# Optimization experiments

Measured on AMD Instinct MI355X. Metric: run time of the kernel, lower is better.

## Reference

```python
import jax, jax.numpy as jnp
import numpy as np

NUM_FEATURES = 128
NUM_FILTERS = 128

def setup_inputs() -> dict:
    key = jax.random.key(0)
    k1, k2, k3, k4, k5 = jax.random.split(key, 5)
    B, N, F = 4, 2048, NUM_FEATURES
    x = jax.random.normal(k1, (B, N, F), dtype=jnp.float32)
    A = jax.random.normal(k2, (B, N, N), dtype=jnp.float32)
    # Conv1D(num_filters, kernel_size=1, use_bias=False) == per-node linear F -> filters
    W = jax.random.normal(k3, (F, NUM_FILTERS), dtype=jnp.float32) * (1.0 / np.sqrt(F))
    # self.a: Conv1D(1, kernel_size=1) with bias == linear filters -> 1 (shared for x_i and x_j)
    a_w = jax.random.normal(k4, (NUM_FILTERS, 1), dtype=jnp.float32) * (1.0 / np.sqrt(NUM_FILTERS))
    a_b = jax.random.normal(k5, (1,), dtype=jnp.float32) * 0.01
    bias = jnp.zeros((NUM_FILTERS,), dtype=jnp.float32)
    return {"x": x, "A": A, "W": W, "a_w": a_w, "a_b": a_b, "bias": bias}

def reference(x, A, W, a_w, a_b, bias):
    # project features: [B,N,F] @ [F,Ff] -> [B,N,Ff]
    h = jnp.einsum('bnf,fg->bng', x, W)
    # shared attention projection (x_i and x_j use the same layer): [B,N,1]
    s = jnp.einsum('bng,go->bno', h, a_w) + a_b
    # additive scores s_i + s_j^T -> [B,N,N]
    e = s + jnp.swapaxes(s, 1, 2)
    e = jnp.where(e >= 0, e, 0.2 * e)  # LeakyReLU(0.2)
    attn = jax.nn.softmax(e + A, axis=-1)
    out = jnp.einsum('bij,bjg->big', attn, h) + bias
    return out
```

## Files before the change

kernel.cpp:

```cpp
#include <hip/hip_runtime.h>
#include <hip/hip_bf16.h>
#include <stdint.h>

#define BB 4
#define NN 2048
#define FF 128

typedef __attribute__((ext_vector_type(8))) short bf16x8;
typedef __attribute__((ext_vector_type(4))) float f32x4;

__device__ inline unsigned pk_bf16(float a, float b) {
    union { float f; unsigned u; } x, y;
    x.f = a; y.f = b;
    unsigned xu = x.u + (0x7fffu + ((x.u >> 16) & 1u));
    unsigned yu = y.u + (0x7fffu + ((y.u >> 16) & 1u));
    return (xu >> 16) | (yu & 0xffff0000u);
}

#define XT_P 136
#define WT_P 136

__global__ __launch_bounds__(256) void k1_proj(
    const float* __restrict__ x, const float* __restrict__ W,
    const float* __restrict__ a_w, const float* __restrict__ a_b,
    uint16_t* __restrict__ Ht, float* __restrict__ s_out)
{
    __shared__ uint16_t xt[16 * XT_P];
    __shared__ uint16_t Wt[128 * WT_P];
    __shared__ float sredw[4 * 16];

    const int t = threadIdx.x;
    const int w = t >> 6, l = t & 63;
    const int m16 = l & 15, q = l >> 4;
    const int b = blockIdx.x >> 7;
    const int n0 = (blockIdx.x & 127) << 4;

    const int c4 = (t & 31) * 4, kh = (t >> 5) * 16;
    float4 wr0[8], wr1[8];
    #pragma unroll
    for (int kk = 0; kk < 8; ++kk) {
        const int k = kh + 2 * kk;
        wr0[kk] = *(const float4*)(W + (size_t)k * 128 + c4);
        wr1[kk] = *(const float4*)(W + (size_t)(k + 1) * 128 + c4);
    }
    {
        const int row = t >> 4, c0 = (t & 15) * 8;
        const float* xr = x + ((size_t)(b * NN + n0 + row)) * FF + c0;
        const float4 v0 = *(const float4*)xr;
        const float4 v1 = *(const float4*)(xr + 4);
        unsigned* dst = (unsigned*)(xt + row * XT_P + c0);
        dst[0] = pk_bf16(v0.x, v0.y); dst[1] = pk_bf16(v0.z, v0.w);
        dst[2] = pk_bf16(v1.x, v1.y); dst[3] = pk_bf16(v1.z, v1.w);
    }
    #pragma unroll
    for (int kk = 0; kk < 8; ++kk) {
        const int k = kh + 2 * kk;
        *(unsigned*)(Wt + (c4 + 0) * WT_P + k) = pk_bf16(wr0[kk].x, wr1[kk].x);
        *(unsigned*)(Wt + (c4 + 1) * WT_P + k) = pk_bf16(wr0[kk].y, wr1[kk].y);
        *(unsigned*)(Wt + (c4 + 2) * WT_P + k) = pk_bf16(wr0[kk].z, wr1[kk].z);
        *(unsigned*)(Wt + (c4 + 3) * WT_P + k) = pk_bf16(wr0[kk].w, wr1[kk].w);
    }
    const int g0 = (2 * w) * 16 + m16, g1 = (2 * w + 1) * 16 + m16;
    const float aw0 = a_w[g0], aw1 = a_w[g1];
    __syncthreads();

    f32x4 acc0 = {}, acc1 = {};
    bf16x8 af[4];
    #pragma unroll
    for (int dk = 0; dk < 4; ++dk)
        af[dk] = *(const bf16x8*)(xt + m16 * XT_P + dk * 32 + q * 8);
    #pragma unroll
    for (int dk = 0; dk < 4; ++dk) {
        bf16x8 b0 = *(const bf16x8*)(Wt + g0 * WT_P + dk * 32 + q * 8);
        bf16x8 b1 = *(const bf16x8*)(Wt + g1 * WT_P + dk * 32 + q * 8);
        acc0 = __builtin_amdgcn_mfma_f32_16x16x32_bf16(af[dk], b0, acc0, 0, 0, 0);
        acc1 = __builtin_amdgcn_mfma_f32_16x16x32_bf16(af[dk], b1, acc1, 0, 0, 0);
    }

    float sp[4];
    #pragma unroll
    for (int r = 0; r < 4; ++r) sp[r] = acc0[r] * aw0 + acc1[r] * aw1;
    #pragma unroll
    for (int off = 1; off < 16; off <<= 1)
        #pragma unroll
        for (int r = 0; r < 4; ++r) sp[r] += __shfl_xor(sp[r], off, 64);
    if (m16 == 0) {
        #pragma unroll
        for (int r = 0; r < 4; ++r) sredw[w * 16 + q * 4 + r] = sp[r];
    }
    {
        uint2 o0 = { pk_bf16(acc0[0], acc0[1]), pk_bf16(acc0[2], acc0[3]) };
        uint2 o1 = { pk_bf16(acc1[0], acc1[1]), pk_bf16(acc1[2], acc1[3]) };
        *(uint2*)(Ht + ((size_t)(b * 128 + g0)) * NN + n0 + q * 4) = o0;
        *(uint2*)(Ht + ((size_t)(b * 128 + g1)) * NN + n0 + q * 4) = o1;
    }
    __syncthreads();
    if (t < 16)
        s_out[b * NN + n0 + t] = sredw[t] + sredw[16 + t] + sredw[32 + t] + sredw[48 + t] + a_b[0];
}

__global__ __launch_bounds__(256, 2) void k2_attn(
    const float* __restrict__ A, const uint16_t* __restrict__ Ht,
    const float* __restrict__ s, const float* __restrict__ bias,
    float* __restrict__ out)
{
    __shared__ float Opw[4][16 * 132];
    __shared__ float rsw[4][16];

    const int t = threadIdx.x;
    const int w = t >> 6, l = t & 63;
    const int m16 = l & 15, q = l >> 4;

    const int is = blockIdx.x & 127;
    const int b  = blockIdx.x >> 7;
    const int ibase = is * 16;

    const float* sb = s + b * NN;
    const float* Ab = A + (size_t)b * NN * NN;
    const uint16_t* Hb = Ht + (size_t)b * FF * NN;

    const float si = sb[ibase + m16];
    const float* Ar = Ab + (size_t)(ibase + m16) * NN;

    const int co = w * 32 + q * 8;

    float4 a00 = *(const float4*)(Ar + co);
    float4 a01 = *(const float4*)(Ar + co + 4);
    float4 a10 = *(const float4*)(Ar + co + 128);
    float4 a11 = *(const float4*)(Ar + co + 132);
    float4 sj00 = *(const float4*)(sb + co);
    float4 sj01 = *(const float4*)(sb + co + 4);
    float4 sj10 = *(const float4*)(sb + co + 128);
    float4 sj11 = *(const float4*)(sb + co + 132);

    f32x4 acc[8];
    #pragma unroll
    for (int gt = 0; gt < 8; ++gt) acc[gt] = (f32x4){0.f, 0.f, 0.f, 0.f};
    float rs = 0.f;

    #pragma unroll
    for (int r = 0; r < 8; ++r) {
        const int jc0 = r * 256 + co;
        const int jc1 = jc0 + 128;

        bf16x8 hf0[8], hf1[8];
        #pragma unroll
        for (int gt = 0; gt < 8; ++gt) {
            const uint16_t* hp = Hb + (size_t)(gt * 16 + m16) * NN;
            hf0[gt] = *(const bf16x8*)(hp + jc0);
            hf1[gt] = *(const bf16x8*)(hp + jc1);
        }

        float4 n00, n01, n10, n11, t00, t01, t10, t11;
        if (r < 7) {
            const int jn = jc0 + 256;
            n00 = *(const float4*)(Ar + jn);
            n01 = *(const float4*)(Ar + jn + 4);
            n10 = *(const float4*)(Ar + jn + 128);
            n11 = *(const float4*)(Ar + jn + 132);
            t00 = *(const float4*)(sb + jn);
            t01 = *(const float4*)(sb + jn + 4);
            t10 = *(const float4*)(sb + jn + 128);
            t11 = *(const float4*)(sb + jn + 132);
        }

        const float svv[16] = {sj00.x,sj00.y,sj00.z,sj00.w, sj01.x,sj01.y,sj01.z,sj01.w,
                               sj10.x,sj10.y,sj10.z,sj10.w, sj11.x,sj11.y,sj11.z,sj11.w};
        const float avv[16] = {a00.x,a00.y,a00.z,a00.w, a01.x,a01.y,a01.z,a01.w,
                               a10.x,a10.y,a10.z,a10.w, a11.x,a11.y,a11.z,a11.w};
        float pv[16];
        #pragma unroll
        for (int j = 0; j < 16; ++j) {
            float e = si + svv[j];
            e = fmaxf(e, 0.2f * e);
            pv[j] = __expf(e + avv[j]);
            rs += pv[j];
        }
        union { unsigned u[4]; bf16x8 v; } fa0, fa1;
        #pragma unroll
        for (int j = 0; j < 4; ++j) {
            fa0.u[j] = pk_bf16(pv[2 * j], pv[2 * j + 1]);
            fa1.u[j] = pk_bf16(pv[8 + 2 * j], pv[9 + 2 * j]);
        }

        #pragma unroll
        for (int gt = 0; gt < 8; ++gt) {
            acc[gt] = __builtin_amdgcn_mfma_f32_16x16x32_bf16(fa0.v, hf0[gt], acc[gt], 0, 0, 0);
            acc[gt] = __builtin_amdgcn_mfma_f32_16x16x32_bf16(fa1.v, hf1[gt], acc[gt], 0, 0, 0);
        }

        if (r < 7) {
            a00 = n00; a01 = n01; a10 = n10; a11 = n11;
            sj00 = t00; sj01 = t01; sj10 = t10; sj11 = t11;
        }
    }

    rs += __shfl_xor(rs, 16, 64);
    rs += __shfl_xor(rs, 32, 64);
    if (q == 0) rsw[w][m16] = rs;
    #pragma unroll
    for (int gt = 0; gt < 8; ++gt)
        #pragma unroll
        for (int rr = 0; rr < 4; ++rr)
            Opw[w][(q * 4 + rr) * 132 + gt * 16 + m16] = acc[gt][rr];
    __syncthreads();

    {
        const int row = t >> 4, k8 = (t & 15) * 8;
        float v[8] = {0.f,0.f,0.f,0.f,0.f,0.f,0.f,0.f};
        #pragma unroll
        for (int sl = 0; sl < 4; ++sl) {
            float4 u0 = *(const float4*)&Opw[sl][row * 132 + k8];
            float4 u1 = *(const float4*)&Opw[sl][row * 132 + k8 + 4];
            v[0] += u0.x; v[1] += u0.y; v[2] += u0.z; v[3] += u0.w;
            v[4] += u1.x; v[5] += u1.y; v[6] += u1.z; v[7] += u1.w;
        }
        const float rst = rsw[0][row] + rsw[1][row] + rsw[2][row] + rsw[3][row];
        const float inv = 1.0f / rst;
        const float4 b0 = *(const float4*)(bias + k8);
        const float4 b1 = *(const float4*)(bias + k8 + 4);
        float4 o0 = { v[0]*inv + b0.x, v[1]*inv + b0.y, v[2]*inv + b0.z, v[3]*inv + b0.w };
        float4 o1 = { v[4]*inv + b1.x, v[5]*inv + b1.y, v[6]*inv + b1.z, v[7]*inv + b1.w };
        float* op = out + ((size_t)(b * NN + ibase + row)) * FF + k8;
        *(float4*)op = o0;
        *(float4*)(op + 4) = o1;
    }
}

extern "C" void kernel_launch(void* const* d_in, const int* in_sizes, int n_in,
                              void* d_out, int out_size, void* d_ws, size_t ws_size,
                              hipStream_t stream) {
    const float* x    = (const float*)d_in[0];
    const float* A    = (const float*)d_in[1];
    const float* W    = (const float*)d_in[2];
    const float* a_w  = (const float*)d_in[3];
    const float* a_b  = (const float*)d_in[4];
    const float* bias = (const float*)d_in[5];
    float* out = (float*)d_out;

    char* ws = (char*)d_ws;
    uint16_t* Ht = (uint16_t*)ws;
    float* s = (float*)(ws + 2 * 1024 * 1024);

    k1_proj<<<BB * (NN / 16), 256, 0, stream>>>(x, W, a_w, a_b, Ht, s);
    k2_attn<<<128 * BB, 256, 0, stream>>>(A, Ht, s, bias, out);
}
```

Baseline: 138.7 us.

## Split attention K-loop across eight waves per block with two-stage LDS reduction

The attention kernel now runs 512 threads (8 waves) per block, and each wave handles one 8-column chunk per 256-column stripe instead of two, halving per-wave registers and loop work. The explicit software prefetch of A and s is dropped, the block index is remapped so that batches are interleaved, and partial outputs are reduced through LDS in two phases (upper waves store, lower waves accumulate) so the buffer size stays the same. The aim is more waves in flight to hide the latency of streaming A. The cost is an extra barrier and the loss of explicit prefetching.

```diff
diff --git a/kernel.cpp b/kernel.cpp
--- a/kernel.cpp
+++ b/kernel.cpp
@@ -99,20 +99,20 @@
         s_out[b * NN + n0 + t] = sredw[t] + sredw[16 + t] + sredw[32 + t] + sredw[48 + t] + a_b[0];
 }
 
-__global__ __launch_bounds__(256, 2) void k2_attn(
+__global__ __launch_bounds__(512, 4) void k2_attn(
     const float* __restrict__ A, const uint16_t* __restrict__ Ht,
     const float* __restrict__ s, const float* __restrict__ bias,
     float* __restrict__ out)
 {
     __shared__ float Opw[4][16 * 132];
-    __shared__ float rsw[4][16];
+    __shared__ float rsw[8][16];
 
     const int t = threadIdx.x;
     const int w = t >> 6, l = t & 63;
     const int m16 = l & 15, q = l >> 4;
 
-    const int is = blockIdx.x & 127;
-    const int b  = blockIdx.x >> 7;
+    const int b  = blockIdx.x & 3;
+    const int is = blockIdx.x >> 2;
     const int ibase = is * 16;
 
     const float* sb = s + b * NN;
@@ -121,17 +121,9 @@
 
     const float si = sb[ibase + m16];
     const float* Ar = Ab + (size_t)(ibase + m16) * NN;
+    const uint16_t* Hr = Hb + (size_t)m16 * NN;
 
     const int co = w * 32 + q * 8;
-
-    float4 a00 = *(const float4*)(Ar + co);
-    float4 a01 = *(const float4*)(Ar + co + 4);
-    float4 a10 = *(const float4*)(Ar + co + 128);
-    float4 a11 = *(const float4*)(Ar + co + 132);
-    float4 sj00 = *(const float4*)(sb + co);
-    float4 sj01 = *(const float4*)(sb + co + 4);
-    float4 sj10 = *(const float4*)(sb + co + 128);
-    float4 sj11 = *(const float4*)(sb + co + 132);
 
     f32x4 acc[8];
     #pragma unroll
@@ -139,91 +131,76 @@
     float rs = 0.f;
 
     #pragma unroll
-    for (int r = 0; r < 8; ++r) {
-        const int jc0 = r * 256 + co;
-        const int jc1 = jc0 + 128;
-
-        bf16x8 hf0[8], hf1[8];
-        #pragma unroll
-        for (int gt = 0; gt < 8; ++gt) {
-            const uint16_t* hp = Hb + (size_t)(gt * 16 + m16) * NN;
-            hf0[gt] = *(const bf16x8*)(hp + jc0);
-            hf1[gt] = *(const bf16x8*)(hp + jc1);
-        }
-
-        float4 n00, n01, n10, n11, t00, t01, t10, t11;
-        if (r < 7) {
-            const int jn = jc0 + 256;
-            n00 = *(const float4*)(Ar + jn);
-            n01 = *(const float4*)(Ar + jn + 4);
-            n10 = *(const float4*)(Ar + jn + 128);
-            n11 = *(const float4*)(Ar + jn + 132);
-            t00 = *(const float4*)(sb + jn);
-            t01 = *(const float4*)(sb + jn + 4);
-            t10 = *(const float4*)(sb + jn + 128);
-            t11 = *(const float4*)(sb + jn + 132);
-        }
-
-        const float svv[16] = {sj00.x,sj00.y,sj00.z,sj00.w, sj01.x,sj01.y,sj01.z,sj01.w,
-                               sj10.x,sj10.y,sj10.z,sj10.w, sj11.x,sj11.y,sj11.z,sj11.w};
-        const float avv[16] = {a00.x,a00.y,a00.z,a00.w, a01.x,a01.y,a01.z,a01.w,
-                               a10.x,a10.y,a10.z,a10.w, a11.x,a11.y,a11.z,a11.w};
-        float pv[16];
-        #pragma unroll
-        for (int j = 0; j < 16; ++j) {
-            float e = si + svv[j];
+    for (int hr = 0; hr < 8; ++hr) {
+        const int jc = hr * 256 + co;
+
+        bf16x8 hf[8];
+        #pragma unroll
+        for (int gt = 0; gt < 8; ++gt)
+            hf[gt] = *(const bf16x8*)(Hr + (size_t)(gt * 16) * NN + jc);
+
+        float4 a0 = *(const float4*)(Ar + jc);
+        float4 a1 = *(const float4*)(Ar + jc + 4);
+        float4 s0 = *(const float4*)(sb + jc);
+        float4 s1 = *(const float4*)(sb + jc + 4);
+
+        const float sv[8] = {s0.x, s0.y, s0.z, s0.w, s1.x, s1.y, s1.z, s1.w};
+        const float av[8] = {a0.x, a0.y, a0.z, a0.w, a1.x, a1.y, a1.z, a1.w};
+        float pv[8];
+        #pragma unroll
+        for (int j = 0; j < 8; ++j) {
+            float e = si + sv[j];
             e = fmaxf(e, 0.2f * e);
-            pv[j] = __expf(e + avv[j]);
+            pv[j] = __expf(e + av[j]);
             rs += pv[j];
         }
-        union { unsigned u[4]; bf16x8 v; } fa0, fa1;
-        #pragma unroll
-        for (int j = 0; j < 4; ++j) {
-            fa0.u[j] = pk_bf16(pv[2 * j], pv[2 * j + 1]);
-            fa1.u[j] = pk_bf16(pv[8 + 2 * j], pv[9 + 2 * j]);
-        }
-
-        #pragma unroll
-        for (int gt = 0; gt < 8; ++gt) {
-            acc[gt] = __builtin_amdgcn_mfma_f32_16x16x32_bf16(fa0.v, hf0[gt], acc[gt], 0, 0, 0);
-            acc[gt] = __builtin_amdgcn_mfma_f32_16x16x32_bf16(fa1.v, hf1[gt], acc[gt], 0, 0, 0);
-        }
-
-        if (r < 7) {
-            a00 = n00; a01 = n01; a10 = n10; a11 = n11;
-            sj00 = t00; sj01 = t01; sj10 = t10; sj11 = t11;
-        }
+        union { unsigned u[4]; bf16x8 v; } fa;
+        #pragma unroll
+        for (int j = 0; j < 4; ++j)
+            fa.u[j] = pk_bf16(pv[2 * j], pv[2 * j + 1]);
+
+        #pragma unroll
+        for (int gt = 0; gt < 8; ++gt)
+            acc[gt] = __builtin_amdgcn_mfma_f32_16x16x32_bf16(fa.v, hf[gt], acc[gt], 0, 0, 0);
     }
 
     rs += __shfl_xor(rs, 16, 64);
     rs += __shfl_xor(rs, 32, 64);
     if (q == 0) rsw[w][m16] = rs;
-    #pragma unroll
-    for (int gt = 0; gt < 8; ++gt)
-        #pragma unroll
-        for (int rr = 0; rr < 4; ++rr)
-            Opw[w][(q * 4 + rr) * 132 + gt * 16 + m16] = acc[gt][rr];
+
+    if (w >= 4) {
+        #pragma unroll
+        for (int gt = 0; gt < 8; ++gt)
+            #pragma unroll
+            for (int rr = 0; rr < 4; ++rr)
+                Opw[w - 4][(q * 4 + rr) * 132 + gt * 16 + m16] = acc[gt][rr];
+    }
+    __syncthreads();
+    if (w < 4) {
+        #pragma unroll
+        for (int gt = 0; gt < 8; ++gt)
+            #pragma unroll
+            for (int rr = 0; rr < 4; ++rr)
+                Opw[w][(q * 4 + rr) * 132 + gt * 16 + m16] += acc[gt][rr];
+    }
     __syncthreads();
 
     {
-        const int row = t >> 4, k8 = (t & 15) * 8;
-        float v[8] = {0.f,0.f,0.f,0.f,0.f,0.f,0.f,0.f};
+        const int row = t >> 5, k4 = (t & 31) * 4;
+        float4 v = {0.f, 0.f, 0.f, 0.f};
         #pragma unroll
         for (int sl = 0; sl < 4; ++sl) {
-            float4 u0 = *(const float4*)&Opw[sl][row * 132 + k8];
-            float4 u1 = *(const float4*)&Opw[sl][row * 132 + k8 + 4];
-            v[0] += u0.x; v[1] += u0.y; v[2] += u0.z; v[3] += u0.w;
-            v[4] += u1.x; v[5] += u1.y; v[6] += u1.z; v[7] += u1.w;
+            float4 u = *(const float4*)&Opw[sl][row * 132 + k4];
+            v.x += u.x; v.y += u.y; v.z += u.z; v.w += u.w;
         }
-        const float rst = rsw[0][row] + rsw[1][row] + rsw[2][row] + rsw[3][row];
+        float rst = 0.f;
+        #pragma unroll
+        for (int sl = 0; sl < 8; ++sl) rst += rsw[sl][row];
         const float inv = 1.0f / rst;
-        const float4 b0 = *(const float4*)(bias + k8);
-        const float4 b1 = *(const float4*)(bias + k8 + 4);
-        float4 o0 = { v[0]*inv + b0.x, v[1]*inv + b0.y, v[2]*inv + b0.z, v[3]*inv + b0.w };
-        float4 o1 = { v[4]*inv + b1.x, v[5]*inv + b1.y, v[6]*inv + b1.z, v[7]*inv + b1.w };
-        float* op = out + ((size_t)(b * NN + ibase + row)) * FF + k8;
-        *(float4*)op = o0;
-        *(float4*)(op + 4) = o1;
+        const float4 bv = *(const float4*)(bias + k4);
+        float4 o = { v.x * inv + bv.x, v.y * inv + bv.y,
+                     v.z * inv + bv.z, v.w * inv + bv.w };
+        *(float4*)(out + ((size_t)(b * NN + ibase + row)) * FF + k4) = o;
     }
 }
 
@@ -243,5 +220,5 @@
     float* s = (float*)(ws + 2 * 1024 * 1024);
 
     k1_proj<<<BB * (NN / 16), 256, 0, stream>>>(x, W, a_w, a_b, Ht, s);
-    k2_attn<<<128 * BB, 256, 0, stream>>>(A, Ht, s, bias, out);
-}
+    k2_attn<<<512, 512, 0, stream>>>(A, Ht, s, bias, out);
+}
```

Result: slower. 147.6 us (+6.5%).
